# Performance work log

Measured on AMD Instinct MI355X. Metric: run time of the kernel, lower is better.

The kernel has to match this reference:

```python
import jax, jax.numpy as jnp
import numpy as np

B, S, D, H = 2, 2048, 1024, 16
DEPTH = D // H


def setup_inputs() -> dict:
    key = jax.random.key(0)
    ks = jax.random.split(key, 12)
    scale = 1.0 / np.sqrt(D)
    inp = {
        "v": jax.random.normal(ks[0], (B, S, D), jnp.float32),
        "k": jax.random.normal(ks[1], (B, S, D), jnp.float32),
        "q": jax.random.normal(ks[2], (B, S, D), jnp.float32),
        "mask": jnp.tril(jnp.ones((S, S), jnp.int32))[None, None],  # causal [1,1,S,S]
        "wq_w": jax.random.normal(ks[3], (D, D), jnp.float32) * scale,
        "wq_b": jnp.zeros((D,), jnp.float32),
        "wk_w": jax.random.normal(ks[4], (D, D), jnp.float32) * scale,
        "wk_b": jnp.zeros((D,), jnp.float32),
        "wv_w": jax.random.normal(ks[5], (D, D), jnp.float32) * scale,
        "wv_b": jnp.zeros((D,), jnp.float32),
        "dense_w": jax.random.normal(ks[6], (D, D), jnp.float32) * scale,
        "dense_b": jnp.zeros((D,), jnp.float32),
    }
    return inp


def _split_heads(x):
    # [B, S, D] -> [B, H, S, depth]
    b, s, _ = x.shape
    return x.reshape(b, s, H, DEPTH).transpose(0, 2, 1, 3)


def reference(v, k, q, mask, wq_w, wq_b, wk_w, wk_b, wv_w, wv_b, dense_w, dense_b):
    qh = _split_heads(q @ wq_w.T + wq_b)
    kh = _split_heads(k @ wk_w.T + wk_b)
    vh = _split_heads(v @ wv_w.T + wv_b)
    scores = jnp.einsum("bhqd,bhkd->bhqk", qh, kh) / jnp.sqrt(jnp.float32(DEPTH))
    scores = jnp.where(mask == 0, jnp.float32(-1e9), scores)
    attn = jax.nn.softmax(scores, axis=-1)
    out = jnp.einsum("bhqk,bhkd->bhqd", attn, vh)
    out = out.transpose(0, 2, 1, 3).reshape(q.shape[0], -1, D)
    out = out @ dense_w.T + dense_b
    return (out, attn)
```

## Files before the change

kernel.cpp:

```cpp
#include <hip/hip_runtime.h>
#include <hip/hip_bf16.h>
#include <stdint.h>

#define S_LEN 2048
#define D_DIM 1024
#define NH    16
#define DEPTH 64
#define NB    2

typedef __attribute__((ext_vector_type(8))) short bf16x8;
typedef __attribute__((ext_vector_type(4))) float f32x4;

static __device__ __forceinline__ unsigned short f2b(float f) {
  union { float f; uint32_t u; } v; v.f = f;
  uint32_t u = v.u;
  uint32_t r = (u + 0x7FFFu + ((u >> 16) & 1u)) >> 16;
  return (unsigned short)r;
}

static __device__ __forceinline__ void gload_lds16(const void* g, void* l) {
  __builtin_amdgcn_global_load_lds(
      (const __attribute__((address_space(1))) uint32_t*)g,
      (__attribute__((address_space(3))) uint32_t*)l, 16, 0, 0);
}

#define SWZ(off, row) ((off) ^ (((row) & 7u) << 4))

struct CvtArgs {
  const float* src[7];
  unsigned short* dst[7];
  int n[7];
};

__global__ __launch_bounds__(256) void cvt_kernel(CvtArgs a) {
  const int z = blockIdx.y;
  const float* __restrict__ s = a.src[z];
  unsigned short* __restrict__ d = a.dst[z];
  const int n8 = a.n[z] >> 3;
  const int stride = gridDim.x * 256;
  for (int i = blockIdx.x * 256 + threadIdx.x; i < n8; i += stride) {
    const float4* sp = (const float4*)(s + (size_t)i * 8);
    float4 x = sp[0], y = sp[1];
    union { unsigned short u[8]; uint4 v; } o;
    o.u[0] = f2b(x.x); o.u[1] = f2b(x.y); o.u[2] = f2b(x.z); o.u[3] = f2b(x.w);
    o.u[4] = f2b(y.x); o.u[5] = f2b(y.y); o.u[6] = f2b(y.z); o.u[7] = f2b(y.w);
    *(uint4*)(d + (size_t)i * 8) = o.v;
  }
}

struct GemmArgs {
  const unsigned short* A[3];
  const unsigned short* Bw[3];
  const float* bias[3];
  void* C[3];
  int M, N, K;
  int out_f32;
};

__global__ __launch_bounds__(256) void gemm_bt_kernel(GemmArgs g) {
  const int z = blockIdx.z;
  const unsigned short* __restrict__ A = g.A[z];
  const unsigned short* __restrict__ Bw = g.Bw[z];
  const float* __restrict__ bias = g.bias[z];
  const int K = g.K, N = g.N;
  const int tid = threadIdx.x, lane = tid & 63, wave = tid >> 6;
  const int wr = wave >> 1, wc = wave & 1;
  const int l15 = lane & 15, l4 = lane >> 4;
  const int brow = blockIdx.y * 128, bcol = blockIdx.x * 128;

  __shared__ unsigned short lsA[128 * 64];
  __shared__ unsigned short lsB[128 * 64];

  f32x4 acc[4][4];
#pragma unroll
  for (int i = 0; i < 4; ++i)
#pragma unroll
    for (int j = 0; j < 4; ++j) acc[i][j] = (f32x4){0.f, 0.f, 0.f, 0.f};

  for (int kt = 0; kt < K; kt += 64) {
    __syncthreads();
#pragma unroll
    for (int i = 0; i < 4; ++i) {
      int c = tid + i * 256;
      int row = c >> 3;
      int lb = (int)(SWZ((uint32_t)(c * 16), (uint32_t)row) & 127u);
      gload_lds16(A + (size_t)(brow + row) * K + kt + (lb >> 1),
                  (char*)lsA + (size_t)c * 16);
      gload_lds16(Bw + (size_t)(bcol + row) * K + kt + (lb >> 1),
                  (char*)lsB + (size_t)c * 16);
    }
    __syncthreads();
#pragma unroll
    for (int kc = 0; kc < 2; ++kc) {
      bf16x8 af[4], bfr[4];
#pragma unroll
      for (int mf = 0; mf < 4; ++mf) {
        uint32_t r = (uint32_t)(wr * 64 + mf * 16 + l15);
        uint32_t off = r * 128 + (uint32_t)(kc * 64 + l4 * 16);
        af[mf] = *(const bf16x8*)((const char*)lsA + SWZ(off, r));
      }
#pragma unroll
      for (int nf = 0; nf < 4; ++nf) {
        uint32_t r = (uint32_t)(wc * 64 + nf * 16 + l15);
        uint32_t off = r * 128 + (uint32_t)(kc * 64 + l4 * 16);
        bfr[nf] = *(const bf16x8*)((const char*)lsB + SWZ(off, r));
      }
#pragma unroll
      for (int mf = 0; mf < 4; ++mf)
#pragma unroll
        for (int nf = 0; nf < 4; ++nf)
          acc[mf][nf] = __builtin_amdgcn_mfma_f32_16x16x32_bf16(
              af[mf], bfr[nf], acc[mf][nf], 0, 0, 0);
    }
  }

  const int of32 = g.out_f32;
#pragma unroll
  for (int nf = 0; nf < 4; ++nf) {
    int gcol = bcol + wc * 64 + nf * 16 + l15;
    float bv = bias[gcol];
#pragma unroll
    for (int mf = 0; mf < 4; ++mf) {
#pragma unroll
      for (int r = 0; r < 4; ++r) {
        int grow = brow + wr * 64 + mf * 16 + l4 * 4 + r;
        float vv = acc[mf][nf][r] + bv;
        if (of32)
          ((float*)g.C[z])[(size_t)grow * N + gcol] = vv;
        else
          ((unsigned short*)g.C[z])[(size_t)grow * N + gcol] = f2b(vv);
      }
    }
  }
}

__global__ __launch_bounds__(256) void vt_kernel(
    const unsigned short* __restrict__ Vp, unsigned short* __restrict__ Vt) {
  const int sc = blockIdx.x, bh = blockIdx.y;
  const int b = bh >> 4, h = bh & 15;
  const int tid = threadIdx.x;
  __shared__ unsigned short t[64][65];

#pragma unroll
  for (int i = 0; i < 2; ++i) {
    int row = (tid >> 3) + i * 32;
    int ch = tid & 7;
    bf16x8 v = *(const bf16x8*)(Vp + ((size_t)(b * S_LEN + sc * 64 + row)) * D_DIM +
                                h * DEPTH + ch * 8);
#pragma unroll
    for (int j = 0; j < 8; ++j) t[row][ch * 8 + j] = (unsigned short)v[j];
  }
  __syncthreads();
#pragma unroll
  for (int i = 0; i < 2; ++i) {
    int d = (tid >> 3) + i * 32;
    int ch = tid & 7;
    union { unsigned short u[8]; uint4 v; } o;
#pragma unroll
    for (int j = 0; j < 8; ++j) o.u[j] = t[ch * 8 + j][d];
    *(uint4*)(Vt + ((size_t)bh * DEPTH + d) * S_LEN + sc * 64 + ch * 8) = o.v;
  }
}

__global__ __launch_bounds__(256) void flash_kernel(
    const unsigned short* __restrict__ Qp, const unsigned short* __restrict__ Kp,
    const unsigned short* __restrict__ Vt, float* __restrict__ stats,
    unsigned short* __restrict__ ctx) {
  const int bh = blockIdx.x;
  const int b = bh >> 4, h = bh & 15;
  const int rt = (int)gridDim.y - 1 - (int)blockIdx.y;
  const int tid = threadIdx.x, lane = tid & 63, w = tid >> 6;
  const int l15 = lane & 15, l4 = lane >> 4;
  const int myrow0 = w * 16 + l4 * 4;

  __shared__ unsigned short lsQ[64 * 64];
  __shared__ unsigned short lsK[64 * 64];
  __shared__ unsigned short lsV[64 * 64];
  __shared__ unsigned short lsP[64 * 64];

  const size_t base = (size_t)b * S_LEN * D_DIM + (size_t)h * DEPTH;
  const size_t vbase = (size_t)bh * DEPTH * S_LEN;

#pragma unroll
  for (int i = 0; i < 2; ++i) {
    int c = tid + i * 256;
    int row = c >> 3;
    int lb = (int)(SWZ((uint32_t)(c * 16), (uint32_t)row) & 127u);
    gload_lds16(Qp + base + (size_t)(rt * 64 + row) * D_DIM + (lb >> 1),
                (char*)lsQ + (size_t)c * 16);
  }
  __syncthreads();
  bf16x8 qf[2];
#pragma unroll
  for (int kc = 0; kc < 2; ++kc) {
    uint32_t r = (uint32_t)(w * 16 + l15);
    uint32_t off = r * 128 + (uint32_t)(kc * 64 + l4 * 16);
    qf[kc] = *(const bf16x8*)((const char*)lsQ + SWZ(off, r));
  }

  float l_run[4] = {0.f, 0.f, 0.f, 0.f};
  f32x4 oacc[4];
#pragma unroll
  for (int df = 0; df < 4; ++df) oacc[df] = (f32x4){0.f, 0.f, 0.f, 0.f};

  for (int ct = 0; ct <= rt; ++ct) {
    __syncthreads();
#pragma unroll
    for (int i = 0; i < 2; ++i) {
      int c = tid + i * 256;
      int row = c >> 3;
      int lb = (int)(SWZ((uint32_t)(c * 16), (uint32_t)row) & 127u);
      gload_lds16(Kp + base + (size_t)(ct * 64 + row) * D_DIM + (lb >> 1),
                  (char*)lsK + (size_t)c * 16);
      gload_lds16(Vt + vbase + (size_t)row * S_LEN + ct * 64 + (lb >> 1),
                  (char*)lsV + (size_t)c * 16);
    }
    __syncthreads();
    f32x4 sacc[4];
#pragma unroll
    for (int nf = 0; nf < 4; ++nf) sacc[nf] = (f32x4){0.f, 0.f, 0.f, 0.f};
#pragma unroll
    for (int kc = 0; kc < 2; ++kc) {
#pragma unroll
      for (int nf = 0; nf < 4; ++nf) {
        uint32_t r = (uint32_t)(nf * 16 + l15);
        uint32_t off = r * 128 + (uint32_t)(kc * 64 + l4 * 16);
        bf16x8 kf = *(const bf16x8*)((const char*)lsK + SWZ(off, r));
        sacc[nf] = __builtin_amdgcn_mfma_f32_16x16x32_bf16(qf[kc], kf, sacc[nf], 0, 0, 0);
      }
    }
    const bool diag = (ct == rt);
    float st[4] = {0.f, 0.f, 0.f, 0.f};
#pragma unroll
    for (int nf = 0; nf < 4; ++nf) {
      int gcol = ct * 64 + nf * 16 + l15;
#pragma unroll
      for (int r = 0; r < 4; ++r) {
        int lrow = myrow0 + r;
        float p = (diag && gcol > rt * 64 + lrow)
                      ? 0.f
                      : __expf(sacc[nf][r] * 0.125f);
        st[r] += p;
        uint32_t off = (uint32_t)lrow * 128 + (uint32_t)(nf * 16 + l15) * 2;
        *(unsigned short*)((char*)lsP + SWZ(off, (uint32_t)lrow)) = f2b(p);
      }
    }
#pragma unroll
    for (int r = 0; r < 4; ++r) {
#pragma unroll
      for (int o = 1; o < 16; o <<= 1) st[r] += __shfl_xor(st[r], o);
      l_run[r] += st[r];
    }
#pragma unroll
    for (int kc = 0; kc < 2; ++kc) {
      uint32_t pr = (uint32_t)(w * 16 + l15);
      uint32_t poff = pr * 128 + (uint32_t)(kc * 64 + l4 * 16);
      bf16x8 pa = *(const bf16x8*)((const char*)lsP + SWZ(poff, pr));
#pragma unroll
      for (int df = 0; df < 4; ++df) {
        uint32_t vr = (uint32_t)(df * 16 + l15);
        uint32_t voff = vr * 128 + (uint32_t)(kc * 64 + l4 * 16);
        bf16x8 vb = *(const bf16x8*)((const char*)lsV + SWZ(voff, vr));
        oacc[df] = __builtin_amdgcn_mfma_f32_16x16x32_bf16(pa, vb, oacc[df], 0, 0, 0);
      }
    }
  }

  float invl[4];
#pragma unroll
  for (int r = 0; r < 4; ++r) invl[r] = 1.f / l_run[r];

  if (l15 == 0) {
#pragma unroll
    for (int r = 0; r < 4; ++r)
      stats[(size_t)bh * S_LEN + rt * 64 + myrow0 + r] = invl[r];
  }

#pragma unroll
  for (int df = 0; df < 4; ++df) {
#pragma unroll
    for (int r = 0; r < 4; ++r) {
      int lrow = myrow0 + r;
      int gd = df * 16 + l15;
      ctx[((size_t)b * S_LEN + rt * 64 + lrow) * D_DIM + h * DEPTH + gd] =
          f2b(oacc[df][r] * invl[r]);
    }
  }
}

__global__ __launch_bounds__(256) void attn_write_kernel(
    const unsigned short* __restrict__ Qp, const unsigned short* __restrict__ Kp,
    const float* __restrict__ stats, float* __restrict__ attn_out) {
  const int ct = blockIdx.x, rt = blockIdx.y, bh = blockIdx.z;
  const int tid = threadIdx.x;
  float* attn_tb = attn_out + ((size_t)bh * S_LEN + (size_t)rt * 64) * S_LEN +
                   (size_t)ct * 64;

  if (ct > rt) {
    float4 z4 = {0.f, 0.f, 0.f, 0.f};
#pragma unroll
    for (int i = 0; i < 4; ++i) {
      int f = tid + i * 256;
      int row = f >> 4, cq = f & 15;
      *(float4*)(attn_tb + (size_t)row * S_LEN + cq * 4) = z4;
    }
    return;
  }

  const int b = bh >> 4, h = bh & 15;
  const int lane = tid & 63, w = tid >> 6;
  const int l15 = lane & 15, l4 = lane >> 4;
  const int myrow0 = w * 16 + l4 * 4;

  __shared__ unsigned short lsQ[64 * 64];
  __shared__ unsigned short lsK[64 * 64];
  __shared__ float lsT[64][68];

  const size_t base = (size_t)b * S_LEN * D_DIM + (size_t)h * DEPTH;
#pragma unroll
  for (int i = 0; i < 2; ++i) {
    int c = tid + i * 256;
    int row = c >> 3;
    int lb = (int)(SWZ((uint32_t)(c * 16), (uint32_t)row) & 127u);
    gload_lds16(Qp + base + (size_t)(rt * 64 + row) * D_DIM + (lb >> 1),
                (char*)lsQ + (size_t)c * 16);
    gload_lds16(Kp + base + (size_t)(ct * 64 + row) * D_DIM + (lb >> 1),
                (char*)lsK + (size_t)c * 16);
  }
  __syncthreads();

  bf16x8 qf[2];
#pragma unroll
  for (int kc = 0; kc < 2; ++kc) {
    uint32_t r = (uint32_t)(w * 16 + l15);
    uint32_t off = r * 128 + (uint32_t)(kc * 64 + l4 * 16);
    qf[kc] = *(const bf16x8*)((const char*)lsQ + SWZ(off, r));
  }
  f32x4 sacc[4];
#pragma unroll
  for (int nf = 0; nf < 4; ++nf) sacc[nf] = (f32x4){0.f, 0.f, 0.f, 0.f};
#pragma unroll
  for (int kc = 0; kc < 2; ++kc) {
#pragma unroll
    for (int nf = 0; nf < 4; ++nf) {
      uint32_t r = (uint32_t)(nf * 16 + l15);
      uint32_t off = r * 128 + (uint32_t)(kc * 64 + l4 * 16);
      bf16x8 kf = *(const bf16x8*)((const char*)lsK + SWZ(off, r));
      sacc[nf] = __builtin_amdgcn_mfma_f32_16x16x32_bf16(qf[kc], kf, sacc[nf], 0, 0, 0);
    }
  }

  const float4 invl4 =
      *(const float4*)&stats[(size_t)bh * S_LEN + rt * 64 + myrow0];
  const bool diag = (ct == rt);
#pragma unroll
  for (int nf = 0; nf < 4; ++nf) {
    int col = nf * 16 + l15;
#pragma unroll
    for (int r = 0; r < 4; ++r) {
      int lrow = myrow0 + r;
      float p = (diag && col > lrow)
                    ? 0.f
                    : __expf(sacc[nf][r] * 0.125f) * ((const float*)&invl4)[r];
      lsT[lrow][col] = p;
    }
  }
  __syncthreads();
#pragma unroll
  for (int i = 0; i < 4; ++i) {
    int idx = tid + i * 256;
    int row = idx >> 4, c4 = idx & 15;
    *(float4*)(attn_tb + (size_t)row * S_LEN + c4 * 4) = *(float4*)&lsT[row][c4 * 4];
  }
}

extern "C" void kernel_launch(void* const* d_in, const int* in_sizes, int n_in,
                              void* d_out, int out_size, void* d_ws, size_t ws_size,
                              hipStream_t stream) {
  const float* v_in = (const float*)d_in[0];
  const float* k_in = (const float*)d_in[1];
  const float* q_in = (const float*)d_in[2];
  const float* wq_w = (const float*)d_in[4];
  const float* wq_b = (const float*)d_in[5];
  const float* wk_w = (const float*)d_in[6];
  const float* wk_b = (const float*)d_in[7];
  const float* wv_w = (const float*)d_in[8];
  const float* wv_b = (const float*)d_in[9];
  const float* wd_w = (const float*)d_in[10];
  const float* wd_b = (const float*)d_in[11];

  char* ws = (char*)d_ws;
  const size_t MB = 1024 * 1024;
  unsigned short* q_bf = (unsigned short*)(ws + 0 * MB);
  unsigned short* k_bf = (unsigned short*)(ws + 8 * MB);
  unsigned short* v_bf = (unsigned short*)(ws + 16 * MB);
  unsigned short* wq_bf = (unsigned short*)(ws + 24 * MB);
  unsigned short* wk_bf = (unsigned short*)(ws + 26 * MB);
  unsigned short* wv_bf = (unsigned short*)(ws + 28 * MB);
  unsigned short* wd_bf = (unsigned short*)(ws + 30 * MB);
  unsigned short* Qp = (unsigned short*)(ws + 32 * MB);
  unsigned short* Kp = (unsigned short*)(ws + 40 * MB);
  unsigned short* Vp = (unsigned short*)(ws + 48 * MB);
  float* stats = (float*)(ws + 56 * MB);
  unsigned short* Vt = (unsigned short*)(ws + 58 * MB);
  unsigned short* ctx = (unsigned short*)(ws + 0 * MB);

  float* out = (float*)d_out;
  float* attn = out + (size_t)NB * S_LEN * D_DIM;

  const int n_qkv = NB * S_LEN * D_DIM;
  const int n_w = D_DIM * D_DIM;

  CvtArgs ca;
  ca.src[0] = q_in;  ca.dst[0] = q_bf;  ca.n[0] = n_qkv;
  ca.src[1] = k_in;  ca.dst[1] = k_bf;  ca.n[1] = n_qkv;
  ca.src[2] = v_in;  ca.dst[2] = v_bf;  ca.n[2] = n_qkv;
  ca.src[3] = wq_w;  ca.dst[3] = wq_bf; ca.n[3] = n_w;
  ca.src[4] = wk_w;  ca.dst[4] = wk_bf; ca.n[4] = n_w;
  ca.src[5] = wv_w;  ca.dst[5] = wv_bf; ca.n[5] = n_w;
  ca.src[6] = wd_w;  ca.dst[6] = wd_bf; ca.n[6] = n_w;
  cvt_kernel<<<dim3(1024, 7), dim3(256), 0, stream>>>(ca);

  GemmArgs gq;
  gq.A[0] = q_bf; gq.Bw[0] = wq_bf; gq.bias[0] = wq_b; gq.C[0] = Qp;
  gq.A[1] = k_bf; gq.Bw[1] = wk_bf; gq.bias[1] = wk_b; gq.C[1] = Kp;
  gq.A[2] = v_bf; gq.Bw[2] = wv_bf; gq.bias[2] = wv_b; gq.C[2] = Vp;
  gq.M = NB * S_LEN; gq.N = D_DIM; gq.K = D_DIM; gq.out_f32 = 0;
  gemm_bt_kernel<<<dim3(D_DIM / 128, NB * S_LEN / 128, 3), dim3(256), 0, stream>>>(gq);

  vt_kernel<<<dim3(S_LEN / 64, NB * NH), dim3(256), 0, stream>>>(Vp, Vt);

  flash_kernel<<<dim3(NB * NH, S_LEN / 64), dim3(256), 0, stream>>>(
      Qp, Kp, Vt, stats, ctx);

  attn_write_kernel<<<dim3(S_LEN / 64, S_LEN / 64, NB * NH), dim3(256), 0,
                      stream>>>(Qp, Kp, stats, attn);

  GemmArgs gd;
  gd.A[0] = ctx; gd.Bw[0] = wd_bf; gd.bias[0] = wd_b; gd.C[0] = out;
  gd.A[1] = nullptr; gd.Bw[1] = nullptr; gd.bias[1] = nullptr; gd.C[1] = nullptr;
  gd.A[2] = nullptr; gd.Bw[2] = nullptr; gd.bias[2] = nullptr; gd.C[2] = nullptr;
  gd.M = NB * S_LEN; gd.N = D_DIM; gd.K = D_DIM; gd.out_f32 = 1;
  gemm_bt_kernel<<<dim3(D_DIM / 128, NB * S_LEN / 128, 1), dim3(256), 0, stream>>>(gd);
}
```

Baseline: 761.7 us.

## Fuse V transpose into QKV GEMM epilogue and widen attn-write tiles

The V projection GEMM now writes its output directly in the transposed per-head layout, which removes the separate vt_kernel launch and the round trip through Vp. The attention-probability writer now covers two 64-column tiles per block, loading the Q tile once and reusing it for both K tiles, which halves the grid size. This costs more LDS per block, an extra barrier per tile, and stride-S_LEN 8-byte stores in the V epilogue that may coalesce poorly.

```diff
diff --git a/kernel.cpp b/kernel.cpp
--- a/kernel.cpp
+++ b/kernel.cpp
@@ -53,8 +53,7 @@
   const unsigned short* Bw[3];
   const float* bias[3];
   void* C[3];
-  int M, N, K;
-  int out_f32;
+  int mode[3];
 };
 
 __global__ __launch_bounds__(256) void gemm_bt_kernel(GemmArgs g) {
@@ -62,7 +61,7 @@
   const unsigned short* __restrict__ A = g.A[z];
   const unsigned short* __restrict__ Bw = g.Bw[z];
   const float* __restrict__ bias = g.bias[z];
-  const int K = g.K, N = g.N;
+  const int K = D_DIM, N = D_DIM;
   const int tid = threadIdx.x, lane = tid & 63, wave = tid >> 6;
   const int wr = wave >> 1, wc = wave & 1;
   const int l15 = lane & 15, l4 = lane >> 4;
@@ -114,51 +113,43 @@
     }
   }
 
-  const int of32 = g.out_f32;
-#pragma unroll
-  for (int nf = 0; nf < 4; ++nf) {
-    int gcol = bcol + wc * 64 + nf * 16 + l15;
-    float bv = bias[gcol];
-#pragma unroll
-    for (int mf = 0; mf < 4; ++mf) {
-#pragma unroll
-      for (int r = 0; r < 4; ++r) {
-        int grow = brow + wr * 64 + mf * 16 + l4 * 4 + r;
-        float vv = acc[mf][nf][r] + bv;
-        if (of32)
-          ((float*)g.C[z])[(size_t)grow * N + gcol] = vv;
-        else
-          ((unsigned short*)g.C[z])[(size_t)grow * N + gcol] = f2b(vv);
-      }
-    }
-  }
-}
-
-__global__ __launch_bounds__(256) void vt_kernel(
-    const unsigned short* __restrict__ Vp, unsigned short* __restrict__ Vt) {
-  const int sc = blockIdx.x, bh = blockIdx.y;
-  const int b = bh >> 4, h = bh & 15;
-  const int tid = threadIdx.x;
-  __shared__ unsigned short t[64][65];
-
-#pragma unroll
-  for (int i = 0; i < 2; ++i) {
-    int row = (tid >> 3) + i * 32;
-    int ch = tid & 7;
-    bf16x8 v = *(const bf16x8*)(Vp + ((size_t)(b * S_LEN + sc * 64 + row)) * D_DIM +
-                                h * DEPTH + ch * 8);
-#pragma unroll
-    for (int j = 0; j < 8; ++j) t[row][ch * 8 + j] = (unsigned short)v[j];
-  }
-  __syncthreads();
-#pragma unroll
-  for (int i = 0; i < 2; ++i) {
-    int d = (tid >> 3) + i * 32;
-    int ch = tid & 7;
-    union { unsigned short u[8]; uint4 v; } o;
-#pragma unroll
-    for (int j = 0; j < 8; ++j) o.u[j] = t[ch * 8 + j][d];
-    *(uint4*)(Vt + ((size_t)bh * DEPTH + d) * S_LEN + sc * 64 + ch * 8) = o.v;
+  const int mode = g.mode[z];
+  if (mode == 2) {
+    unsigned short* Vt = (unsigned short*)g.C[z];
+#pragma unroll
+    for (int nf = 0; nf < 4; ++nf) {
+      int gcol = bcol + wc * 64 + nf * 16 + l15;
+      float bv = bias[gcol];
+      int h = gcol >> 6, dd = gcol & 63;
+#pragma unroll
+      for (int mf = 0; mf < 4; ++mf) {
+        int grow0 = brow + wr * 64 + mf * 16 + l4 * 4;
+        int bb = grow0 >> 11, s0 = grow0 & 2047;
+        union { unsigned short u[4]; uint2 v; } pk;
+#pragma unroll
+        for (int r = 0; r < 4; ++r) pk.u[r] = f2b(acc[mf][nf][r] + bv);
+        *(uint2*)(Vt + (((size_t)(bb * NH + h) * DEPTH + dd) * S_LEN + s0)) =
+            pk.v;
+      }
+    }
+  } else {
+#pragma unroll
+    for (int nf = 0; nf < 4; ++nf) {
+      int gcol = bcol + wc * 64 + nf * 16 + l15;
+      float bv = bias[gcol];
+#pragma unroll
+      for (int mf = 0; mf < 4; ++mf) {
+#pragma unroll
+        for (int r = 0; r < 4; ++r) {
+          int grow = brow + wr * 64 + mf * 16 + l4 * 4 + r;
+          float vv = acc[mf][nf][r] + bv;
+          if (mode)
+            ((float*)g.C[z])[(size_t)grow * N + gcol] = vv;
+          else
+            ((unsigned short*)g.C[z])[(size_t)grow * N + gcol] = f2b(vv);
+        }
+      }
+    }
   }
 }
 
@@ -291,18 +282,18 @@
 __global__ __launch_bounds__(256) void attn_write_kernel(
     const unsigned short* __restrict__ Qp, const unsigned short* __restrict__ Kp,
     const float* __restrict__ stats, float* __restrict__ attn_out) {
-  const int ct = blockIdx.x, rt = blockIdx.y, bh = blockIdx.z;
+  const int ct0 = blockIdx.x * 2, rt = blockIdx.y, bh = blockIdx.z;
   const int tid = threadIdx.x;
-  float* attn_tb = attn_out + ((size_t)bh * S_LEN + (size_t)rt * 64) * S_LEN +
-                   (size_t)ct * 64;
-
-  if (ct > rt) {
+  float* attn_rb = attn_out + ((size_t)bh * S_LEN + (size_t)rt * 64) * S_LEN;
+
+  if (ct0 > rt) {
     float4 z4 = {0.f, 0.f, 0.f, 0.f};
-#pragma unroll
-    for (int i = 0; i < 4; ++i) {
+    float* tb = attn_rb + (size_t)ct0 * 64;
+#pragma unroll
+    for (int i = 0; i < 8; ++i) {
       int f = tid + i * 256;
-      int row = f >> 4, cq = f & 15;
-      *(float4*)(attn_tb + (size_t)row * S_LEN + cq * 4) = z4;
+      int row = f >> 5, cq = f & 31;
+      *(float4*)(tb + (size_t)row * S_LEN + cq * 4) = z4;
     }
     return;
   }
@@ -311,9 +302,10 @@
   const int lane = tid & 63, w = tid >> 6;
   const int l15 = lane & 15, l4 = lane >> 4;
   const int myrow0 = w * 16 + l4 * 4;
+  const bool have1 = (ct0 + 1 <= rt);
 
   __shared__ unsigned short lsQ[64 * 64];
-  __shared__ unsigned short lsK[64 * 64];
+  __shared__ unsigned short lsK[2][64 * 64];
   __shared__ float lsT[64][68];
 
   const size_t base = (size_t)b * S_LEN * D_DIM + (size_t)h * DEPTH;
@@ -324,8 +316,11 @@
     int lb = (int)(SWZ((uint32_t)(c * 16), (uint32_t)row) & 127u);
     gload_lds16(Qp + base + (size_t)(rt * 64 + row) * D_DIM + (lb >> 1),
                 (char*)lsQ + (size_t)c * 16);
-    gload_lds16(Kp + base + (size_t)(ct * 64 + row) * D_DIM + (lb >> 1),
-                (char*)lsK + (size_t)c * 16);
+    gload_lds16(Kp + base + (size_t)(ct0 * 64 + row) * D_DIM + (lb >> 1),
+                (char*)lsK[0] + (size_t)c * 16);
+    if (have1)
+      gload_lds16(Kp + base + (size_t)((ct0 + 1) * 64 + row) * D_DIM + (lb >> 1),
+                  (char*)lsK[1] + (size_t)c * 16);
   }
   __syncthreads();
 
@@ -336,41 +331,58 @@
     uint32_t off = r * 128 + (uint32_t)(kc * 64 + l4 * 16);
     qf[kc] = *(const bf16x8*)((const char*)lsQ + SWZ(off, r));
   }
-  f32x4 sacc[4];
-#pragma unroll
-  for (int nf = 0; nf < 4; ++nf) sacc[nf] = (f32x4){0.f, 0.f, 0.f, 0.f};
-#pragma unroll
-  for (int kc = 0; kc < 2; ++kc) {
-#pragma unroll
-    for (int nf = 0; nf < 4; ++nf) {
-      uint32_t r = (uint32_t)(nf * 16 + l15);
-      uint32_t off = r * 128 + (uint32_t)(kc * 64 + l4 * 16);
-      bf16x8 kf = *(const bf16x8*)((const char*)lsK + SWZ(off, r));
-      sacc[nf] = __builtin_amdgcn_mfma_f32_16x16x32_bf16(qf[kc], kf, sacc[nf], 0, 0, 0);
-    }
-  }
-
   const float4 invl4 =
       *(const float4*)&stats[(size_t)bh * S_LEN + rt * 64 + myrow0];
-  const bool diag = (ct == rt);
-#pragma unroll
-  for (int nf = 0; nf < 4; ++nf) {
-    int col = nf * 16 + l15;
-#pragma unroll
-    for (int r = 0; r < 4; ++r) {
-      int lrow = myrow0 + r;
-      float p = (diag && col > lrow)
-                    ? 0.f
-                    : __expf(sacc[nf][r] * 0.125f) * ((const float*)&invl4)[r];
-      lsT[lrow][col] = p;
-    }
-  }
-  __syncthreads();
-#pragma unroll
-  for (int i = 0; i < 4; ++i) {
-    int idx = tid + i * 256;
-    int row = idx >> 4, c4 = idx & 15;
-    *(float4*)(attn_tb + (size_t)row * S_LEN + c4 * 4) = *(float4*)&lsT[row][c4 * 4];
+
+  for (int t = 0; t < 2; ++t) {
+    const int ct = ct0 + t;
+    float* attn_tb = attn_rb + (size_t)ct * 64;
+    if (t == 1 && !have1) {
+      float4 z4 = {0.f, 0.f, 0.f, 0.f};
+#pragma unroll
+      for (int i = 0; i < 4; ++i) {
+        int idx = tid + i * 256;
+        int row = idx >> 4, c4 = idx & 15;
+        *(float4*)(attn_tb + (size_t)row * S_LEN + c4 * 4) = z4;
+      }
+      break;
+    }
+    f32x4 sacc[4];
+#pragma unroll
+    for (int nf = 0; nf < 4; ++nf) sacc[nf] = (f32x4){0.f, 0.f, 0.f, 0.f};
+#pragma unroll
+    for (int kc = 0; kc < 2; ++kc) {
+#pragma unroll
+      for (int nf = 0; nf < 4; ++nf) {
+        uint32_t r = (uint32_t)(nf * 16 + l15);
+        uint32_t off = r * 128 + (uint32_t)(kc * 64 + l4 * 16);
+        bf16x8 kf = *(const bf16x8*)((const char*)lsK[t] + SWZ(off, r));
+        sacc[nf] =
+            __builtin_amdgcn_mfma_f32_16x16x32_bf16(qf[kc], kf, sacc[nf], 0, 0, 0);
+      }
+    }
+    const bool diag = (ct == rt);
+#pragma unroll
+    for (int nf = 0; nf < 4; ++nf) {
+      int col = nf * 16 + l15;
+#pragma unroll
+      for (int r = 0; r < 4; ++r) {
+        int lrow = myrow0 + r;
+        float p = (diag && col > lrow)
+                      ? 0.f
+                      : __expf(sacc[nf][r] * 0.125f) * ((const float*)&invl4)[r];
+        lsT[lrow][col] = p;
+      }
+    }
+    __syncthreads();
+#pragma unroll
+    for (int i = 0; i < 4; ++i) {
+      int idx = tid + i * 256;
+      int row = idx >> 4, c4 = idx & 15;
+      *(float4*)(attn_tb + (size_t)row * S_LEN + c4 * 4) =
+          *(float4*)&lsT[row][c4 * 4];
+    }
+    __syncthreads();
   }
 }
 
@@ -400,7 +412,6 @@
   unsigned short* wd_bf = (unsigned short*)(ws + 30 * MB);
   unsigned short* Qp = (unsigned short*)(ws + 32 * MB);
   unsigned short* Kp = (unsigned short*)(ws + 40 * MB);
-  unsigned short* Vp = (unsigned short*)(ws + 48 * MB);
   float* stats = (float*)(ws + 56 * MB);
   unsigned short* Vt = (unsigned short*)(ws + 58 * MB);
   unsigned short* ctx = (unsigned short*)(ws + 0 * MB);
@@ -422,24 +433,20 @@
   cvt_kernel<<<dim3(1024, 7), dim3(256), 0, stream>>>(ca);
 
   GemmArgs gq;
-  gq.A[0] = q_bf; gq.Bw[0] = wq_bf; gq.bias[0] = wq_b; gq.C[0] = Qp;
-  gq.A[1] = k_bf; gq.Bw[1] = wk_bf; gq.bias[1] = wk_b; gq.C[1] = Kp;
-  gq.A[2] = v_bf; gq.Bw[2] = wv_bf; gq.bias[2] = wv_b; gq.C[2] = Vp;
-  gq.M = NB * S_LEN; gq.N = D_DIM; gq.K = D_DIM; gq.out_f32 = 0;
+  gq.A[0] = q_bf; gq.Bw[0] = wq_bf; gq.bias[0] = wq_b; gq.C[0] = Qp; gq.mode[0] = 0;
+  gq.A[1] = k_bf; gq.Bw[1] = wk_bf; gq.bias[1] = wk_b; gq.C[1] = Kp; gq.mode[1] = 0;
+  gq.A[2] = v_bf; gq.Bw[2] = wv_bf; gq.bias[2] = wv_b; gq.C[2] = Vt; gq.mode[2] = 2;
   gemm_bt_kernel<<<dim3(D_DIM / 128, NB * S_LEN / 128, 3), dim3(256), 0, stream>>>(gq);
-
-  vt_kernel<<<dim3(S_LEN / 64, NB * NH), dim3(256), 0, stream>>>(Vp, Vt);
 
   flash_kernel<<<dim3(NB * NH, S_LEN / 64), dim3(256), 0, stream>>>(
       Qp, Kp, Vt, stats, ctx);
 
-  attn_write_kernel<<<dim3(S_LEN / 64, S_LEN / 64, NB * NH), dim3(256), 0,
+  attn_write_kernel<<<dim3(S_LEN / 128, S_LEN / 64, NB * NH), dim3(256), 0,
                       stream>>>(Qp, Kp, stats, attn);
 
   GemmArgs gd;
-  gd.A[0] = ctx; gd.Bw[0] = wd_bf; gd.bias[0] = wd_b; gd.C[0] = out;
-  gd.A[1] = nullptr; gd.Bw[1] = nullptr; gd.bias[1] = nullptr; gd.C[1] = nullptr;
-  gd.A[2] = nullptr; gd.Bw[2] = nullptr; gd.bias[2] = nullptr; gd.C[2] = nullptr;
-  gd.M = NB * S_LEN; gd.N = D_DIM; gd.K = D_DIM; gd.out_f32 = 1;
+  gd.A[0] = ctx; gd.Bw[0] = wd_bf; gd.bias[0] = wd_b; gd.C[0] = out; gd.mode[0] = 1;
+  gd.A[1] = nullptr; gd.Bw[1] = nullptr; gd.bias[1] = nullptr; gd.C[1] = nullptr; gd.mode[1] = 1;
+  gd.A[2] = nullptr; gd.Bw[2] = nullptr; gd.bias[2] = nullptr; gd.C[2] = nullptr; gd.mode[2] = 1;
   gemm_bt_kernel<<<dim3(D_DIM / 128, NB * S_LEN / 128, 1), dim3(256), 0, stream>>>(gd);
 }
```

Result: faster. 743.7 us (-2.4%).
